# Kernel optimization log

Measured on AMD Instinct MI355X. Metric: run time of the kernel, lower is better.

## Reference

```python
import jax, jax.numpy as jnp
import numpy as np

N, E, H, FE, FV, L, FL, FO = 20000, 320000, 256, 64, 64, 4, 1024, 1


def setup_inputs() -> dict:
    key = jax.random.key(0)
    ks = jax.random.split(key, 28)
    s = 0.05
    rn = lambda k, shp: jax.random.normal(k, shp, jnp.float32) * s
    inp = {
        'x': jax.random.normal(ks[0], (N, FV), jnp.float32),
        'edge_attr': jax.random.normal(ks[1], (E, FE), jnp.float32),
        'edge_index': jax.random.randint(ks[2], (2, E), 0, N, jnp.int64) if False else jax.random.randint(ks[2], (2, E), 0, N),
        'ew': rn(ks[3], (H, FE)), 'eb': rn(ks[4], (H,)),
        'vw': rn(ks[5], (H, FV)), 'vb': rn(ks[6], (H,)),
        'Le_w': rn(ks[7], (L, H, H)), 'Le_b': rn(ks[8], (L, H)),
        'Lv_w': rn(ks[9], (L, H, H)), 'Lv_b': rn(ks[10], (L, H)),
        'bne_g': jnp.ones((L, H), jnp.float32), 'bne_b': jnp.zeros((L, H), jnp.float32),
        'bnv_g': jnp.ones((L, H), jnp.float32), 'bnv_b': jnp.zeros((L, H), jnp.float32),
        'gru_wih': rn(ks[11], (L, 3 * H, H)), 'gru_whh': rn(ks[12], (L, 3 * H, H)),
        'gru_bih': rn(ks[13], (L, 3 * H)), 'gru_bhh': rn(ks[14], (L, 3 * H)),
        'fin_w': rn(ks[15], (FL, H)), 'fin_b': rn(ks[16], (FL,)),
        'out_w': rn(ks[17], (FO, FL)), 'out_b': rn(ks[18], (FO,)),
    }
    return inp


def _bn(x, g, b):
    # BatchNorm1d, training-mode batch statistics (biased variance), eps=1e-5
    m = x.mean(axis=0)
    v = x.var(axis=0)
    return (x - m) * jax.lax.rsqrt(v + 1e-5) * g + b


def _forward(x, edge_attr, edge_index, ew, eb, vw, vb, Le_w, Le_b, Lv_w, Lv_b,
             bne_g, bne_b, bnv_g, bnv_b, gru_wih, gru_whh, gru_bih, gru_bhh,
             fin_w, fin_b, out_w, out_b):
    n_nodes = x.shape[0]
    num_layers = Le_w.shape[0]
    src, dst = edge_index[0], edge_index[1]
    seg = jnp.concatenate([src, dst])  # each edge contributes to both endpoints
    e_in = edge_attr @ ew.T + eb       # [E, H]
    v_in = x @ vw.T + vb               # [N, H]
    for k in range(num_layers):
        e = e_in @ Le_w[k].T + Le_b[k]
        vp = v_in @ Lv_w[k].T + Lv_b[k]
        ep = jax.nn.relu(_bn(e + vp[src] + vp[dst], bne_g[k], bne_b[k]))  # [E, H]
        # scatter-max of incident edge features into each vertex
        vie = jax.ops.segment_max(jnp.concatenate([ep, ep], axis=0), seg,
                                  num_segments=n_nodes)
        vie = jnp.where(jnp.isfinite(vie), vie, 0.0)  # isolated vertices -> 0
        # single-step GRU: input vie, hidden v_in
        gi = vie @ gru_wih[k].T + gru_bih[k]
        gh = v_in @ gru_whh[k].T + gru_bhh[k]
        ir, iz, ig = jnp.split(gi, 3, axis=1)
        hr, hz, hg = jnp.split(gh, 3, axis=1)
        r = jax.nn.sigmoid(ir + hr)
        z = jax.nn.sigmoid(iz + hz)
        n = jnp.tanh(ig + r * hg)
        h = (1.0 - z) * n + z * v_in
        v_c = jax.nn.relu(_bn(h, bnv_g[k], bnv_b[k]))
        v_in = v_c + v_in
        e_in = ep + e_in
    e_fin = e_in @ fin_w.T + fin_b
    return e_fin @ out_w.T + out_b  # [E, 1]


def reference(x, edge_attr, edge_index, ew, eb, vw, vb, Le_w, Le_b, Lv_w, Lv_b,
              bne_g, bne_b, bnv_g, bnv_b, gru_wih, gru_whh, gru_bih, gru_bhh,
              fin_w, fin_b, out_w, out_b):
    return _forward(x, edge_attr, edge_index, ew, eb, vw, vb, Le_w, Le_b, Lv_w,
                    Lv_b, bne_g, bne_b, bnv_g, bnv_b, gru_wih, gru_whh,
                    gru_bih, gru_bhh, fin_w, fin_b, out_w, out_b)
```

## Files before the change

### kernel.cpp

```cpp
#include <hip/hip_runtime.h>
#include <stdint.h>

constexpr int N  = 20000;
constexpr int E  = 320000;
constexpr int H  = 256;
constexpr int FEAT = 64;
constexpr int NL = 4;
constexpr int FL = 1024;

typedef unsigned short u16;
typedef short bf16x8 __attribute__((ext_vector_type(8)));
typedef float f32x4 __attribute__((ext_vector_type(4)));

__device__ __forceinline__ float bf2f(u16 u) {
    union { uint32_t i; float f; } v; v.i = ((uint32_t)u) << 16; return v.f;
}
__device__ __forceinline__ u16 f2bf(float f) {
    union { uint32_t i; float f; } v; v.f = f;
    uint32_t r = v.i + 0x7FFFu + ((v.i >> 16) & 1u);
    return (u16)(r >> 16);
}
__device__ __forceinline__ float sigmf(float x) { return 1.f / (1.f + __expf(-x)); }
__device__ __forceinline__ float tanhf_(float x) { return 2.f / (1.f + __expf(-2.f * x)) - 1.f; }

__device__ __forceinline__ unsigned int encf(float x) {
    unsigned int u = __float_as_uint(x);
    return (u & 0x80000000u) ? ~u : (u | 0x80000000u);
}
__device__ __forceinline__ float decf(unsigned int k) {
    unsigned int u = (k & 0x80000000u) ? (k ^ 0x80000000u) : ~k;
    return __uint_as_float(u);
}

template <bool W16>
__device__ __forceinline__ bf16x8 ldb(const u16* wb, const float* wf, size_t off) {
    if constexpr (W16) {
        return *(const bf16x8*)(wb + off);
    } else {
        float4 b0 = *(const float4*)(wf + off);
        float4 b1 = *(const float4*)(wf + off + 4);
        bf16x8 r;
        r[0] = (short)f2bf(b0.x); r[1] = (short)f2bf(b0.y);
        r[2] = (short)f2bf(b0.z); r[3] = (short)f2bf(b0.w);
        r[4] = (short)f2bf(b1.x); r[5] = (short)f2bf(b1.y);
        r[6] = (short)f2bf(b1.z); r[7] = (short)f2bf(b1.w);
        return r;
    }
}

__global__ void k_fuse_final(const float* __restrict__ fin_w, const float* __restrict__ fin_b,
                             const float* __restrict__ out_w, const float* __restrict__ out_b,
                             float* __restrict__ w_fo) {
    int h = threadIdx.x;
    float acc = 0.f;
    for (int f = 0; f < FL; ++f) acc = fmaf(out_w[f], fin_w[(size_t)f * H + h], acc);
    w_fo[h] = acc;
    if (h == 0) {
        float b = 0.f;
        for (int f = 0; f < FL; ++f) b = fmaf(out_w[f], fin_b[f], b);
        w_fo[H] = b + out_b[0];
    }
}

__global__ void k_cvt_w(const float* __restrict__ w, u16* __restrict__ o, int n4) {
    int i = blockIdx.x * 256 + threadIdx.x;
    if (i < n4) {
        float4 v = *(const float4*)(w + (size_t)i * 4);
        *(ushort4*)(o + (size_t)i * 4) = make_ushort4(f2bf(v.x), f2bf(v.y), f2bf(v.z), f2bf(v.w));
    }
}

__global__ void k_zero_int(int* __restrict__ p, int n) {
    int i = blockIdx.x * 256 + threadIdx.x;
    if (i < n) p[i] = 0;
}
__global__ void k_zero_f64(double* __restrict__ p, int n) {
    int i = blockIdx.x * 256 + threadIdx.x;
    if (i < n) p[i] = 0.0;
}
__global__ void k_hist2(const int* __restrict__ src, const int* __restrict__ dst,
                        int* __restrict__ curS, int* __restrict__ curD) {
    int e = blockIdx.x * 256 + threadIdx.x;
    if (e < E) { atomicAdd(&curS[src[e]], 1); atomicAdd(&curD[dst[e]], 1); }
}
__global__ void k_scan(int* __restrict__ cur) {
    __shared__ int cs[256];
    int t = threadIdx.x;
    constexpr int CH = (N + 255) / 256;
    int beg = t * CH, end = min(beg + CH, N);
    int s = 0;
    for (int i = beg; i < end; ++i) s += cur[i];
    cs[t] = s;
    __syncthreads();
    for (int off = 1; off < 256; off <<= 1) {
        int v = cs[t];
        int u = (t >= off) ? cs[t - off] : 0;
        __syncthreads();
        cs[t] = v + u;
        __syncthreads();
    }
    int run = (t > 0) ? cs[t - 1] : 0;
    for (int i = beg; i < end; ++i) { int d = cur[i]; cur[i] = run; run += d; }
}
__global__ void k_fill_pair(const int* __restrict__ src, const int* __restrict__ dst,
                            int* __restrict__ curS, int* __restrict__ curD,
                            int4* __restrict__ adjS, int4* __restrict__ adjD) {
    int e = blockIdx.x * 256 + threadIdx.x;
    if (e < E) {
        int s = src[e], d = dst[e];
        int p = atomicAdd(&curS[s], 1); adjS[p] = make_int4(e, s, d, s);
        int q = atomicAdd(&curD[d], 1); adjD[q] = make_int4(e, s, d, d);
    }
}
__global__ void k_fill_u32(unsigned int* __restrict__ p, unsigned int val) {
    size_t i = ((size_t)blockIdx.x * 256 + threadIdx.x) * 4;
    uint4 v = make_uint4(val, val, val, val);
    *(uint4*)(p + i) = v;
}

template <bool W16>
__global__ __launch_bounds__(256, 3) void k_proj_mfma(
    const float* __restrict__ A, const u16* __restrict__ wb, const float* __restrict__ wf,
    const float* __restrict__ bias, u16* __restrict__ C, int M)
{
    __shared__ u16 As[64][72];
    int t = threadIdx.x;
    int row0 = blockIdx.x * 64;
    int r = t >> 2, q = t & 3;
    if (row0 + r < M) {
        const float* gp = A + (size_t)(row0 + r) * FEAT + q * 16;
#pragma unroll
        for (int i = 0; i < 4; ++i) {
            float4 v = *(const float4*)(gp + i * 4);
            *(ushort4*)&As[r][q * 16 + i * 4] = make_ushort4(f2bf(v.x), f2bf(v.y), f2bf(v.z), f2bf(v.w));
        }
    } else {
#pragma unroll
        for (int i = 0; i < 4; ++i) *(ushort4*)&As[r][q * 16 + i * 4] = make_ushort4(0, 0, 0, 0);
    }
    __syncthreads();
    int w = t >> 6, l = t & 63, lane16 = l & 15, quad = l >> 4;
    f32x4 acc[4][4];
#pragma unroll
    for (int i = 0; i < 4; ++i)
#pragma unroll
        for (int j = 0; j < 4; ++j) acc[i][j] = (f32x4){0.f, 0.f, 0.f, 0.f};
#pragma unroll
    for (int k0 = 0; k0 < FEAT; k0 += 32) {
        bf16x8 a[4], b[4];
#pragma unroll
        for (int mt = 0; mt < 4; ++mt)
            a[mt] = *(const bf16x8*)&As[mt * 16 + lane16][k0 + quad * 8];
#pragma unroll
        for (int nt = 0; nt < 4; ++nt)
            b[nt] = ldb<W16>(wb, wf, (size_t)(w * 16 + nt * 64 + lane16) * FEAT + k0 + quad * 8);
#pragma unroll
        for (int mt = 0; mt < 4; ++mt)
#pragma unroll
            for (int nt = 0; nt < 4; ++nt)
                acc[mt][nt] = __builtin_amdgcn_mfma_f32_16x16x32_bf16(a[mt], b[nt], acc[mt][nt], 0, 0, 0);
    }
#pragma unroll
    for (int nt = 0; nt < 4; ++nt) {
        int col = w * 16 + nt * 64 + lane16;
        float bv = bias[col];
#pragma unroll
        for (int mt = 0; mt < 4; ++mt)
#pragma unroll
            for (int reg = 0; reg < 4; ++reg) {
                int row = mt * 16 + quad * 4 + reg;
                if (row0 + row < M)
                    C[(size_t)(row0 + row) * H + col] = f2bf(acc[mt][nt][reg] + bv);
            }
    }
}

template <bool W16>
__global__ __launch_bounds__(256, 2) void k_node_mfma(
    const u16* __restrict__ A, const u16* __restrict__ wb, const float* __restrict__ wf,
    u16* __restrict__ C)
{
    __shared__ u16 As[64][264];
    int t = threadIdx.x;
    int row0 = blockIdx.x * 64;
    int rows = min(64, N - row0);
    int r = t >> 2, q = t & 3;
    if (r < rows) {
        const u16* gp = A + (size_t)(row0 + r) * H + q * 64;
#pragma unroll
        for (int i = 0; i < 16; ++i)
            *(ushort4*)&As[r][q * 64 + i * 4] = *(const ushort4*)(gp + i * 4);
    } else {
#pragma unroll
        for (int i = 0; i < 16; ++i) *(ushort4*)&As[r][q * 64 + i * 4] = make_ushort4(0, 0, 0, 0);
    }
    __syncthreads();
    int w = t >> 6, l = t & 63, lane16 = l & 15, quad = l >> 4;
    f32x4 acc[4][4];
#pragma unroll
    for (int i = 0; i < 4; ++i)
#pragma unroll
        for (int j = 0; j < 4; ++j) acc[i][j] = (f32x4){0.f, 0.f, 0.f, 0.f};
    for (int k0 = 0; k0 < H; k0 += 32) {
        bf16x8 a[4], b[4];
#pragma unroll
        for (int mt = 0; mt < 4; ++mt)
            a[mt] = *(const bf16x8*)&As[mt * 16 + lane16][k0 + quad * 8];
#pragma unroll
        for (int nt = 0; nt < 4; ++nt)
            b[nt] = ldb<W16>(wb, wf, (size_t)(w * 16 + nt * 64 + lane16) * H + k0 + quad * 8);
#pragma unroll
        for (int mt = 0; mt < 4; ++mt)
#pragma unroll
            for (int nt = 0; nt < 4; ++nt)
                acc[mt][nt] = __builtin_amdgcn_mfma_f32_16x16x32_bf16(a[mt], b[nt], acc[mt][nt], 0, 0, 0);
    }
#pragma unroll
    for (int nt = 0; nt < 4; ++nt) {
        int col = w * 16 + nt * 64 + lane16;
#pragma unroll
        for (int mt = 0; mt < 4; ++mt)
#pragma unroll
            for (int reg = 0; reg < 4; ++reg) {
                int row = mt * 16 + quad * 4 + reg;
                if (row < rows)
                    C[(size_t)(row0 + row) * H + col] = f2bf(acc[mt][nt][reg]);
            }
    }
}

template <bool FIRST>
__global__ __launch_bounds__(256, 4) void k_edge_mfma(
    const u16* __restrict__ ein, const u16* __restrict__ wbf,
    const u16* __restrict__ vp, const int4* __restrict__ adj,
    const int* __restrict__ endo,
    unsigned int* __restrict__ vie, double* __restrict__ stats_e,
    const float* __restrict__ scale, const float* __restrict__ shift,
    u16* __restrict__ ein_rw)
{
    __shared__ u16 As[32][264];
    __shared__ u16 Us[32][264];
    __shared__ int s_edge[32];
    __shared__ int s_node[32];
    __shared__ int s_int[32];
    u16 (*praw)[264] = As;

    int t = threadIdx.x;
    int p0 = blockIdx.x * 32;
    if (t < 32) {
        int4 en = adj[p0 + t];
        s_edge[t] = en.x; s_node[t] = en.w;
        if (FIRST) {
            int nd = en.w;
            int st = (nd == 0) ? 0 : endo[nd - 1];
            int ee = endo[nd];
            s_int[t] = (st >= p0) && (ee <= p0 + 32);
        }
    }
    __syncthreads();
    int r = t >> 3, q = t & 7;
    {
        int4 en = adj[p0 + r];
        const u16* gp = ein + (size_t)en.x * H + q * 32;
        const u16* vs = vp + (size_t)en.y * H + q * 32;
        const u16* vd = vp + (size_t)en.z * H + q * 32;
#pragma unroll
        for (int i = 0; i < 8; ++i)
            *(ushort4*)&As[r][q * 32 + i * 4] = *(const ushort4*)(gp + i * 4);
#pragma unroll
        for (int i = 0; i < 8; ++i) {
            ushort4 a4 = *(const ushort4*)(vs + i * 4);
            ushort4 b4 = *(const ushort4*)(vd + i * 4);
            *(ushort4*)&Us[r][q * 32 + i * 4] = make_ushort4(
                f2bf(bf2f(a4.x) + bf2f(b4.x)), f2bf(bf2f(a4.y) + bf2f(b4.y)),
                f2bf(bf2f(a4.z) + bf2f(b4.z)), f2bf(bf2f(a4.w) + bf2f(b4.w)));
        }
    }
    __syncthreads();

    int w = t >> 6, l = t & 63, lane16 = l & 15, quad = l >> 4;
    f32x4 acc[2][4];
#pragma unroll
    for (int i = 0; i < 2; ++i)
#pragma unroll
        for (int j = 0; j < 4; ++j) acc[i][j] = (f32x4){0.f, 0.f, 0.f, 0.f};
    const u16* wb0 = wbf + (size_t)(w * 64 + lane16) * H + quad * 8;
    for (int k0 = 0; k0 < H; k0 += 32) {
        bf16x8 a[2], b[4];
#pragma unroll
        for (int mt = 0; mt < 2; ++mt)
            a[mt] = *(const bf16x8*)&As[mt * 16 + lane16][k0 + quad * 8];
#pragma unroll
        for (int nt = 0; nt < 4; ++nt)
            b[nt] = *(const bf16x8*)(wb0 + (size_t)nt * 16 * H + k0);
#pragma unroll
        for (int mt = 0; mt < 2; ++mt)
#pragma unroll
            for (int nt = 0; nt < 4; ++nt)
                acc[mt][nt] = __builtin_amdgcn_mfma_f32_16x16x32_bf16(a[mt], b[nt], acc[mt][nt], 0, 0, 0);
    }
    __syncthreads();

#pragma unroll
    for (int nt = 0; nt < 4; ++nt) {
        int col = w * 64 + nt * 16 + lane16;
        float s = 0.f, qq = 0.f;
#pragma unroll
        for (int mt = 0; mt < 2; ++mt)
#pragma unroll
            for (int reg = 0; reg < 4; ++reg) {
                int row = mt * 16 + quad * 4 + reg;
                float v = acc[mt][nt][reg] + bf2f(Us[row][col]);
                praw[row][col] = f2bf(v);
                if (FIRST) { s += v; qq += v * v; }
            }
        if (FIRST) {
            s  += __shfl_xor(s, 16, 64);  s  += __shfl_xor(s, 32, 64);
            qq += __shfl_xor(qq, 16, 64); qq += __shfl_xor(qq, 32, 64);
            if (quad == 0) {
                int slice = blockIdx.x & 63;
                atomicAdd(&stats_e[(size_t)slice * 512 + col], (double)s);
                atomicAdd(&stats_e[(size_t)slice * 512 + 256 + col], (double)qq);
            }
        }
    }
    __syncthreads();
    {
        int cur = s_node[0];
        float m = bf2f(praw[0][t]);
        for (int rr = 1; rr < 32; ++rr) {
            int nd = s_node[rr];
            float v = bf2f(praw[rr][t]);
            if (nd != cur) {
                if (FIRST && s_int[rr - 1])
                    vie[(size_t)cur * H + t] = encf(m);
                else
                    atomicMax(&vie[(size_t)cur * H + t], encf(m));
                cur = nd; m = v;
            } else m = fmaxf(m, v);
        }
        if (FIRST && s_int[31])
            vie[(size_t)cur * H + t] = encf(m);
        else
            atomicMax(&vie[(size_t)cur * H + t], encf(m));
    }
    if (!FIRST) {
        u16* gp = ein_rw + (size_t)s_edge[r] * H + q * 32;
        const float* scp = scale + q * 32;
        const float* shp = shift + q * 32;
#pragma unroll
        for (int i = 0; i < 8; ++i) {
            int c = q * 32 + i * 4;
            ushort2 pa = *(const ushort2*)&praw[r][c];
            ushort2 pb = *(const ushort2*)&praw[r][c + 2];
            float4 sc = *(const float4*)(scp + i * 4);
            float4 sh = *(const float4*)(shp + i * 4);
            ushort4 ev = *(const ushort4*)(gp + i * 4);
            float o0 = bf2f(ev.x) + fmaxf(fmaf(bf2f(pa.x), sc.x, sh.x), 0.f);
            float o1 = bf2f(ev.y) + fmaxf(fmaf(bf2f(pa.y), sc.y, sh.y), 0.f);
            float o2 = bf2f(ev.z) + fmaxf(fmaf(bf2f(pb.x), sc.z, sh.z), 0.f);
            float o3 = bf2f(ev.w) + fmaxf(fmaf(bf2f(pb.y), sc.w, sh.w), 0.f);
            *(ushort4*)(gp + i * 4) = make_ushort4(f2bf(o0), f2bf(o1), f2bf(o2), f2bf(o3));
        }
    }
}

__global__ void k_bn_final_e(const double* __restrict__ stats_e,
                             const float* __restrict__ g, const float* __restrict__ b,
                             float* __restrict__ scale, float* __restrict__ shift) {
    int j = threadIdx.x;
    double m = 0.0, q = 0.0;
    for (int s = 0; s < 64; ++s) {
        m += stats_e[(size_t)s * 512 + j];
        q += stats_e[(size_t)s * 512 + 256 + j];
    }
    m /= (double)E;
    double var = q / (double)E - m * m;
    if (var < 0.0) var = 0.0;
    float inv = rsqrtf((float)var + 1e-5f);
    float sc = g[j] * inv;
    scale[j] = sc;
    shift[j] = b[j] - (float)m * sc;
}

__global__ void k_bn_final(const double* __restrict__ stats, int base,
                           const float* __restrict__ g, const float* __restrict__ b,
                           double cnt, float* __restrict__ scale, float* __restrict__ shift) {
    int j = threadIdx.x;
    double m = stats[base + j] / cnt;
    double var = stats[base + 256 + j] / cnt - m * m;
    if (var < 0.0) var = 0.0;
    float inv = rsqrtf((float)var + 1e-5f);
    float sc = g[j] * inv;
    scale[j] = sc;
    shift[j] = b[j] - (float)m * sc;
}

__global__ void k_vie_final(unsigned int* __restrict__ vie_u,
                            const float* __restrict__ scale, const float* __restrict__ shift) {
    size_t idx = ((size_t)blockIdx.x * 256 + threadIdx.x) * 4;
    int col = (int)(idx & (size_t)(H - 1));
    uint4 u = *(const uint4*)(vie_u + idx);
    float4 sc = *(const float4*)(scale + col);
    float4 sh = *(const float4*)(shift + col);
    float4 o;
    o.x = (u.x == 0u) ? 0.f : fmaxf(fmaf(decf(u.x), sc.x, sh.x), 0.f);
    o.y = (u.y == 0u) ? 0.f : fmaxf(fmaf(decf(u.y), sc.y, sh.y), 0.f);
    o.z = (u.z == 0u) ? 0.f : fmaxf(fmaf(decf(u.z), sc.z, sh.z), 0.f);
    o.w = (u.w == 0u) ? 0.f : fmaxf(fmaf(decf(u.w), sc.w, sh.w), 0.f);
    *(float4*)((float*)vie_u + idx) = o;
}

template <bool W16>
__global__ __launch_bounds__(256, 2) void k_gru_mfma(
    const float* __restrict__ vie, const u16* __restrict__ vin,
    const u16* __restrict__ wihb, const float* __restrict__ wihf,
    const u16* __restrict__ whhb, const float* __restrict__ whhf,
    const float* __restrict__ bih, const float* __restrict__ bhh,
    u16* __restrict__ hout, double* __restrict__ stats_v)
{
    __shared__ u16 Ae[64][264];
    __shared__ u16 Av[64][264];
    __shared__ float csum[256], csq[256];
    int t = threadIdx.x;
    int row0 = blockIdx.x * 64;
    int rows = min(64, N - row0);
    int r = t >> 2, q = t & 3;
    if (r < rows) {
        const float* gp = vie + (size_t)(row0 + r) * H + q * 64;
        const u16* hp = vin + (size_t)(row0 + r) * H + q * 64;
#pragma unroll
        for (int i = 0; i < 16; ++i) {
            float4 v = *(const float4*)(gp + i * 4);
            *(ushort4*)&Ae[r][q * 64 + i * 4] = make_ushort4(f2bf(v.x), f2bf(v.y), f2bf(v.z), f2bf(v.w));
            *(ushort4*)&Av[r][q * 64 + i * 4] = *(const ushort4*)(hp + i * 4);
        }
    } else {
#pragma unroll
        for (int i = 0; i < 16; ++i) {
            *(ushort4*)&Ae[r][q * 64 + i * 4] = make_ushort4(0, 0, 0, 0);
            *(ushort4*)&Av[r][q * 64 + i * 4] = make_ushort4(0, 0, 0, 0);
        }
    }
    __syncthreads();
    int w = t >> 6, l = t & 63, lane16 = l & 15, quad = l >> 4;

    for (int g = 0; g < 4; ++g) {
        int j = g * 64 + w * 16 + lane16;
        f32x4 aR[4], aZ[4], aIG[4], aHG[4];
#pragma unroll
        for (int mt = 0; mt < 4; ++mt) {
            aR[mt] = (f32x4){0.f, 0.f, 0.f, 0.f};  aZ[mt] = (f32x4){0.f, 0.f, 0.f, 0.f};
            aIG[mt] = (f32x4){0.f, 0.f, 0.f, 0.f}; aHG[mt] = (f32x4){0.f, 0.f, 0.f, 0.f};
        }
        for (int k0 = 0; k0 < H; k0 += 32) {
            size_t kq = (size_t)k0 + quad * 8;
            bf16x8 ae[4], av[4];
#pragma unroll
            for (int mt = 0; mt < 4; ++mt) {
                ae[mt] = *(const bf16x8*)&Ae[mt * 16 + lane16][k0 + quad * 8];
                av[mt] = *(const bf16x8*)&Av[mt * 16 + lane16][k0 + quad * 8];
            }
            bf16x8 bri = ldb<W16>(wihb, wihf, (size_t)j * H + kq);
            bf16x8 bzi = ldb<W16>(wihb, wihf, (size_t)(H + j) * H + kq);
            bf16x8 bgi = ldb<W16>(wihb, wihf, (size_t)(2 * H + j) * H + kq);
            bf16x8 brh = ldb<W16>(whhb, whhf, (size_t)j * H + kq);
            bf16x8 bzh = ldb<W16>(whhb, whhf, (size_t)(H + j) * H + kq);
            bf16x8 bgh = ldb<W16>(whhb, whhf, (size_t)(2 * H + j) * H + kq);
#pragma unroll
            for (int mt = 0; mt < 4; ++mt) {
                aR[mt]  = __builtin_amdgcn_mfma_f32_16x16x32_bf16(ae[mt], bri, aR[mt], 0, 0, 0);
                aR[mt]  = __builtin_amdgcn_mfma_f32_16x16x32_bf16(av[mt], brh, aR[mt], 0, 0, 0);
                aZ[mt]  = __builtin_amdgcn_mfma_f32_16x16x32_bf16(ae[mt], bzi, aZ[mt], 0, 0, 0);
                aZ[mt]  = __builtin_amdgcn_mfma_f32_16x16x32_bf16(av[mt], bzh, aZ[mt], 0, 0, 0);
                aIG[mt] = __builtin_amdgcn_mfma_f32_16x16x32_bf16(ae[mt], bgi, aIG[mt], 0, 0, 0);
                aHG[mt] = __builtin_amdgcn_mfma_f32_16x16x32_bf16(av[mt], bgh, aHG[mt], 0, 0, 0);
            }
        }
        float br_ = bih[j] + bhh[j];
        float bz_ = bih[H + j] + bhh[H + j];
        float bgi_ = bih[2 * H + j];
        float bgh_ = bhh[2 * H + j];
        float s = 0.f, qq = 0.f;
#pragma unroll
        for (int mt = 0; mt < 4; ++mt)
#pragma unroll
            for (int reg = 0; reg < 4; ++reg) {
                int row = mt * 16 + quad * 4 + reg;
                float rr = sigmf(aR[mt][reg] + br_);
                float zz = sigmf(aZ[mt][reg] + bz_);
                float nn = tanhf_(aIG[mt][reg] + bgi_ + rr * (aHG[mt][reg] + bgh_));
                float vv = bf2f(Av[row][j]);
                float hv = (1.f - zz) * nn + zz * vv;
                if (row < rows) {
                    hout[(size_t)(row0 + row) * H + j] = f2bf(hv);
                    s += hv; qq += hv * hv;
                }
            }
        s  += __shfl_xor(s, 16, 64);  s  += __shfl_xor(s, 32, 64);
        qq += __shfl_xor(qq, 16, 64); qq += __shfl_xor(qq, 32, 64);
        if (quad == 0) { csum[j] = s; csq[j] = qq; }
    }
    __syncthreads();
    atomicAdd(&stats_v[t], (double)csum[t]);
    atomicAdd(&stats_v[256 + t], (double)csq[t]);
}

__global__ void k_vertex_update(u16* __restrict__ vin, const u16* __restrict__ h,
                                const float* __restrict__ scale, const float* __restrict__ shift) {
    size_t idx = ((size_t)blockIdx.x * 256 + threadIdx.x) * 4;
    int col = (int)(idx & (size_t)(H - 1));
    ushort4 hv = *(const ushort4*)(h + idx);
    float4 sc = *(const float4*)(scale + col);
    float4 sh = *(const float4*)(shift + col);
    ushort4 vv = *(const ushort4*)(vin + idx);
    float o0 = bf2f(vv.x) + fmaxf(fmaf(bf2f(hv.x), sc.x, sh.x), 0.f);
    float o1 = bf2f(vv.y) + fmaxf(fmaf(bf2f(hv.y), sc.y, sh.y), 0.f);
    float o2 = bf2f(vv.z) + fmaxf(fmaf(bf2f(hv.z), sc.z, sh.z), 0.f);
    float o3 = bf2f(vv.w) + fmaxf(fmaf(bf2f(hv.w), sc.w, sh.w), 0.f);
    *(ushort4*)(vin + idx) = make_ushort4(f2bf(o0), f2bf(o1), f2bf(o2), f2bf(o3));
}

__global__ __launch_bounds__(256) void k_final(const u16* __restrict__ ein,
                                               const float* __restrict__ w_fo, float* __restrict__ out) {
    int t = threadIdx.x;
    int lane = t & 63;
    int w = (blockIdx.x << 2) + (t >> 6);
    float4 wv = *(const float4*)(w_fo + lane * 4);
    float bfo = w_fo[H];
    int e0 = w * 64;
    for (int e = e0; e < e0 + 64; ++e) {
        ushort4 u = *(const ushort4*)(ein + (size_t)e * H + lane * 4);
        float p = bf2f(u.x) * wv.x + bf2f(u.y) * wv.y + bf2f(u.z) * wv.z + bf2f(u.w) * wv.w;
        for (int off = 32; off > 0; off >>= 1) p += __shfl_down(p, off, 64);
        if (lane == 0) out[e] = p + bfo;
    }
}

template <bool W16>
static void run_all(void* const* d_in, void* d_out, void* d_ws, hipStream_t stream) {
    const float* x         = (const float*)d_in[0];
    const float* edge_attr = (const float*)d_in[1];
    const int*   ei        = (const int*)d_in[2];
    const int*   src = ei;
    const int*   dst = ei + E;
    const float* ew  = (const float*)d_in[3];
    const float* eb  = (const float*)d_in[4];
    const float* vw  = (const float*)d_in[5];
    const float* vb  = (const float*)d_in[6];
    const float* Le_w = (const float*)d_in[7];
    const float* Lv_w = (const float*)d_in[9];
    const float* bne_g = (const float*)d_in[11];
    const float* bne_b = (const float*)d_in[12];
    const float* bnv_g = (const float*)d_in[13];
    const float* bnv_b = (const float*)d_in[14];
    const float* gwih  = (const float*)d_in[15];
    const float* gwhh  = (const float*)d_in[16];
    const float* gbih  = (const float*)d_in[17];
    const float* gbhh  = (const float*)d_in[18];
    const float* fin_w = (const float*)d_in[19];
    const float* fin_b = (const float*)d_in[20];
    const float* out_w = (const float*)d_in[21];
    const float* out_b = (const float*)d_in[22];
    float* out = (float*)d_out;

    const size_t nh = (size_t)N * H, eh = (size_t)E * H;
    char* base = (char*)d_ws;
    size_t off = 0;
    auto alloc = [&](size_t bytes) -> char* {
        char* p = base + off;
        off = (off + bytes + 255) & ~(size_t)255;
        return p;
    };
    float* w_fo = (float*)alloc((H + 1) * sizeof(float));
    u16* v_in = (u16*)alloc(nh * sizeof(u16));
    u16* vp   = (u16*)alloc(nh * sizeof(u16));
    unsigned int* vie_u = (unsigned int*)alloc(nh * sizeof(unsigned int));
    u16* e_in = (u16*)alloc(eh * sizeof(u16));
    u16* wbf  = (u16*)alloc((size_t)NL * H * H * sizeof(u16));
    double* stats_e = (double*)alloc((size_t)64 * 512 * sizeof(double));
    double* stats_v = (double*)alloc(512 * sizeof(double));
    float* scale_e = (float*)alloc(H * sizeof(float));
    float* shift_e = (float*)alloc(H * sizeof(float));
    float* scale_v = (float*)alloc(H * sizeof(float));
    float* shift_v = (float*)alloc(H * sizeof(float));
    int* curS = (int*)alloc((size_t)N * sizeof(int));
    int* curD = (int*)alloc((size_t)N * sizeof(int));
    int4* adjS = (int4*)alloc((size_t)E * sizeof(int4));
    int4* adjD = (int4*)alloc((size_t)E * sizeof(int4));
    u16 *wbf_v = nullptr, *wbf_ih = nullptr, *wbf_hh = nullptr, *ew_b = nullptr, *vw_b = nullptr;
    if (W16) {
        wbf_v  = (u16*)alloc((size_t)NL * H * H * sizeof(u16));
        wbf_ih = (u16*)alloc((size_t)NL * 3 * H * H * sizeof(u16));
        wbf_hh = (u16*)alloc((size_t)NL * 3 * H * H * sizeof(u16));
        ew_b   = (u16*)alloc((size_t)H * FEAT * sizeof(u16));
        vw_b   = (u16*)alloc((size_t)H * FEAT * sizeof(u16));
    }
    u16* hbuf = vp;

    k_fuse_final<<<1, 256, 0, stream>>>(fin_w, fin_b, out_w, out_b, w_fo);
    k_cvt_w<<<(NL * H * H / 4 + 255) / 256, 256, 0, stream>>>(Le_w, wbf, NL * H * H / 4);
    if (W16) {
        k_cvt_w<<<(NL * H * H / 4 + 255) / 256, 256, 0, stream>>>(Lv_w, wbf_v, NL * H * H / 4);
        k_cvt_w<<<(NL * 3 * H * H / 4 + 255) / 256, 256, 0, stream>>>(gwih, wbf_ih, NL * 3 * H * H / 4);
        k_cvt_w<<<(NL * 3 * H * H / 4 + 255) / 256, 256, 0, stream>>>(gwhh, wbf_hh, NL * 3 * H * H / 4);
        k_cvt_w<<<(H * FEAT / 4 + 255) / 256, 256, 0, stream>>>(ew, ew_b, H * FEAT / 4);
        k_cvt_w<<<(H * FEAT / 4 + 255) / 256, 256, 0, stream>>>(vw, vw_b, H * FEAT / 4);
    }
    k_zero_int<<<(N + 255) / 256, 256, 0, stream>>>(curS, N);
    k_zero_int<<<(N + 255) / 256, 256, 0, stream>>>(curD, N);
    k_hist2<<<E / 256, 256, 0, stream>>>(src, dst, curS, curD);
    k_scan<<<1, 256, 0, stream>>>(curS);
    k_scan<<<1, 256, 0, stream>>>(curD);
    k_fill_pair<<<E / 256, 256, 0, stream>>>(src, dst, curS, curD, adjS, adjD);
    const int ntile = (N + 63) / 64;
    k_proj_mfma<W16><<<ntile, 256, 0, stream>>>(x, vw_b, vw, vb, v_in, N);
    k_proj_mfma<W16><<<E / 64, 256, 0, stream>>>(edge_attr, ew_b, ew, eb, e_in, E);

    const int nstat = 64 * 512 + 512;
    for (int k = 0; k < NL; ++k) {
        k_zero_f64<<<(nstat + 255) / 256, 256, 0, stream>>>(stats_e, nstat);
        k_fill_u32<<<(int)(nh / 4 / 256), 256, 0, stream>>>(vie_u, 0u);
        k_node_mfma<W16><<<ntile, 256, 0, stream>>>(v_in,
            W16 ? wbf_v + (size_t)k * H * H : nullptr, Lv_w + (size_t)k * H * H, vp);
        k_edge_mfma<true><<<E / 32, 256, 0, stream>>>(e_in, wbf + (size_t)k * H * H, vp,
                                                      adjD, curD, vie_u, stats_e, nullptr, nullptr, nullptr);
        k_bn_final_e<<<1, 256, 0, stream>>>(stats_e, bne_g + k * H, bne_b + k * H, scale_e, shift_e);
        k_edge_mfma<false><<<E / 32, 256, 0, stream>>>(e_in, wbf + (size_t)k * H * H, vp,
                                                       adjS, curS, vie_u, nullptr, scale_e, shift_e, e_in);
        k_vie_final<<<(int)(nh / 4 / 256), 256, 0, stream>>>(vie_u, scale_e, shift_e);
        k_gru_mfma<W16><<<ntile, 256, 0, stream>>>((const float*)vie_u, v_in,
            W16 ? wbf_ih + (size_t)k * 3 * H * H : nullptr, gwih + (size_t)k * 3 * H * H,
            W16 ? wbf_hh + (size_t)k * 3 * H * H : nullptr, gwhh + (size_t)k * 3 * H * H,
            gbih + (size_t)k * 3 * H, gbhh + (size_t)k * 3 * H, hbuf, stats_v);
        k_bn_final<<<1, 256, 0, stream>>>(stats_v, 0, bnv_g + k * H, bnv_b + k * H, (double)N, scale_v, shift_v);
        k_vertex_update<<<(int)(nh / 4 / 256), 256, 0, stream>>>(v_in, hbuf, scale_v, shift_v);
    }
    k_final<<<E / 256, 256, 0, stream>>>(e_in, w_fo, out);
}

extern "C" void kernel_launch(void* const* d_in, const int* in_sizes, int n_in,
                              void* d_out, int out_size, void* d_ws, size_t ws_size,
                              hipStream_t stream) {
    (void)in_sizes; (void)n_in; (void)out_size;
    const size_t nh = (size_t)N * H, eh = (size_t)E * H;
    auto rup = [](size_t x) { return (x + 255) & ~(size_t)255; };
    size_t need_base = rup((H + 1) * 4) + 2 * rup(nh * 2) + rup(nh * 4) + rup(eh * 2)
                     + rup((size_t)NL * H * H * 2) + rup((size_t)64 * 512 * 8) + rup(512 * 8)
                     + 4 * rup(H * 4) + 2 * rup((size_t)N * 4) + 2 * rup((size_t)E * 16);
    size_t need_w16 = rup((size_t)NL * H * H * 2)
                    + 2 * rup((size_t)NL * 3 * H * H * 2) + 2 * rup((size_t)H * FEAT * 2);
    if (ws_size == 0 || ws_size >= need_base + need_w16)
        run_all<true>(d_in, d_out, d_ws, stream);
    else
        run_all<false>(d_in, d_out, d_ws, stream);
}
```

Baseline: 2.984 ms.

## Store edge features permuted in destination-sorted order for coalesced access

Edge features e_in are now stored in dst-sorted order: the initial projection scatters rows through a permutation, and the first edge pass reads its tiles contiguously instead of gathering by edge id. The second (src-sorted) pass indexes through the permuted position, and the final output kernel scatters results back to original edge order. This removes one random gather per layer in the first pass and drops the separate adjD table, in exchange for a permuted write at projection time and a scattered final output write.

New measurement: 3.030 ms. About the same (+1.5%).

```diff
diff --git a/kernel.cpp b/kernel.cpp
--- a/kernel.cpp
+++ b/kernel.cpp
@@ -7,6 +7,7 @@
 constexpr int FEAT = 64;
 constexpr int NL = 4;
 constexpr int FL = 1024;
+constexpr int NB_E = E / 32;
 
 typedef unsigned short u16;
 typedef short bf16x8 __attribute__((ext_vector_type(8)));
@@ -102,14 +103,17 @@
     int run = (t > 0) ? cs[t - 1] : 0;
     for (int i = beg; i < end; ++i) { int d = cur[i]; cur[i] = run; run += d; }
 }
-__global__ void k_fill_pair(const int* __restrict__ src, const int* __restrict__ dst,
+__global__ void k_fill_perm(const int* __restrict__ src, const int* __restrict__ dst,
                             int* __restrict__ curS, int* __restrict__ curD,
-                            int4* __restrict__ adjS, int4* __restrict__ adjD) {
+                            int4* __restrict__ adjS, int4* __restrict__ sd2, int* __restrict__ pos) {
     int e = blockIdx.x * 256 + threadIdx.x;
     if (e < E) {
         int s = src[e], d = dst[e];
-        int p = atomicAdd(&curS[s], 1); adjS[p] = make_int4(e, s, d, s);
-        int q = atomicAdd(&curD[d], 1); adjD[q] = make_int4(e, s, d, d);
+        int q = atomicAdd(&curD[d], 1);
+        sd2[q] = make_int4(s, d, e, 0);
+        pos[e] = q;
+        int p = atomicAdd(&curS[s], 1);
+        adjS[p] = make_int4(q, s, d, s);
     }
 }
 __global__ void k_fill_u32(unsigned int* __restrict__ p, unsigned int val) {
@@ -121,7 +125,7 @@
 template <bool W16>
 __global__ __launch_bounds__(256, 3) void k_proj_mfma(
     const float* __restrict__ A, const u16* __restrict__ wb, const float* __restrict__ wf,
-    const float* __restrict__ bias, u16* __restrict__ C, int M)
+    const float* __restrict__ bias, u16* __restrict__ C, int M, const int* __restrict__ perm)
 {
     __shared__ u16 As[64][72];
     int t = threadIdx.x;
@@ -169,8 +173,10 @@
 #pragma unroll
             for (int reg = 0; reg < 4; ++reg) {
                 int row = mt * 16 + quad * 4 + reg;
-                if (row0 + row < M)
-                    C[(size_t)(row0 + row) * H + col] = f2bf(acc[mt][nt][reg] + bv);
+                if (row0 + row < M) {
+                    int pr = perm ? perm[row0 + row] : row0 + row;
+                    C[(size_t)pr * H + col] = f2bf(acc[mt][nt][reg] + bv);
+                }
             }
     }
 }
@@ -229,41 +235,26 @@
     }
 }
 
-template <bool FIRST>
-__global__ __launch_bounds__(256, 4) void k_edge_mfma(
-    const u16* __restrict__ ein, const u16* __restrict__ wbf,
-    const u16* __restrict__ vp, const int4* __restrict__ adj,
+__global__ __launch_bounds__(256, 4) void k_edge_first(
+    const u16* __restrict__ ein2, const u16* __restrict__ wbf,
+    const u16* __restrict__ vp, const int4* __restrict__ sd2,
     const int* __restrict__ endo,
-    unsigned int* __restrict__ vie, double* __restrict__ stats_e,
-    const float* __restrict__ scale, const float* __restrict__ shift,
-    u16* __restrict__ ein_rw)
+    unsigned int* __restrict__ vie, double* __restrict__ stats_e)
 {
     __shared__ u16 As[32][264];
     __shared__ u16 Us[32][264];
-    __shared__ int s_edge[32];
     __shared__ int s_node[32];
     __shared__ int s_int[32];
     u16 (*praw)[264] = As;
 
     int t = threadIdx.x;
     int p0 = blockIdx.x * 32;
-    if (t < 32) {
-        int4 en = adj[p0 + t];
-        s_edge[t] = en.x; s_node[t] = en.w;
-        if (FIRST) {
-            int nd = en.w;
-            int st = (nd == 0) ? 0 : endo[nd - 1];
-            int ee = endo[nd];
-            s_int[t] = (st >= p0) && (ee <= p0 + 32);
-        }
-    }
-    __syncthreads();
     int r = t >> 3, q = t & 7;
     {
-        int4 en = adj[p0 + r];
-        const u16* gp = ein + (size_t)en.x * H + q * 32;
-        const u16* vs = vp + (size_t)en.y * H + q * 32;
-        const u16* vd = vp + (size_t)en.z * H + q * 32;
+        int4 en = sd2[p0 + r];
+        const u16* gp = ein2 + (size_t)(p0 + r) * H + q * 32;
+        const u16* vs = vp + (size_t)en.x * H + q * 32;
+        const u16* vd = vp + (size_t)en.y * H + q * 32;
 #pragma unroll
         for (int i = 0; i < 8; ++i)
             *(ushort4*)&As[r][q * 32 + i * 4] = *(const ushort4*)(gp + i * 4);
@@ -276,6 +267,13 @@
                 f2bf(bf2f(a4.z) + bf2f(b4.z)), f2bf(bf2f(a4.w) + bf2f(b4.w)));
         }
     }
+    if (t < 32) {
+        int nd = sd2[p0 + t].y;
+        s_node[t] = nd;
+        int st = (nd == 0) ? 0 : endo[nd - 1];
+        int ee = endo[nd];
+        s_int[t] = (st >= p0) && (ee <= p0 + 32);
+    }
     __syncthreads();
 
     int w = t >> 6, l = t & 63, lane16 = l & 15, quad = l >> 4;
@@ -312,16 +310,14 @@
                 int row = mt * 16 + quad * 4 + reg;
                 float v = acc[mt][nt][reg] + bf2f(Us[row][col]);
                 praw[row][col] = f2bf(v);
-                if (FIRST) { s += v; qq += v * v; }
+                s += v; qq += v * v;
             }
-        if (FIRST) {
-            s  += __shfl_xor(s, 16, 64);  s  += __shfl_xor(s, 32, 64);
-            qq += __shfl_xor(qq, 16, 64); qq += __shfl_xor(qq, 32, 64);
-            if (quad == 0) {
-                int slice = blockIdx.x & 63;
-                atomicAdd(&stats_e[(size_t)slice * 512 + col], (double)s);
-                atomicAdd(&stats_e[(size_t)slice * 512 + 256 + col], (double)qq);
-            }
+        s  += __shfl_xor(s, 16, 64);  s  += __shfl_xor(s, 32, 64);
+        qq += __shfl_xor(qq, 16, 64); qq += __shfl_xor(qq, 32, 64);
+        if (quad == 0) {
+            int slice = blockIdx.x & 63;
+            atomicAdd(&stats_e[(size_t)slice * 512 + col], (double)s);
+            atomicAdd(&stats_e[(size_t)slice * 512 + 256 + col], (double)qq);
         }
     }
     __syncthreads();
@@ -332,20 +328,105 @@
             int nd = s_node[rr];
             float v = bf2f(praw[rr][t]);
             if (nd != cur) {
-                if (FIRST && s_int[rr - 1])
-                    vie[(size_t)cur * H + t] = encf(m);
-                else
-                    atomicMax(&vie[(size_t)cur * H + t], encf(m));
+                if (s_int[rr - 1]) vie[(size_t)cur * H + t] = encf(m);
+                else atomicMax(&vie[(size_t)cur * H + t], encf(m));
                 cur = nd; m = v;
             } else m = fmaxf(m, v);
         }
-        if (FIRST && s_int[31])
-            vie[(size_t)cur * H + t] = encf(m);
-        else
-            atomicMax(&vie[(size_t)cur * H + t], encf(m));
-    }
-    if (!FIRST) {
-        u16* gp = ein_rw + (size_t)s_edge[r] * H + q * 32;
+        if (s_int[31]) vie[(size_t)cur * H + t] = encf(m);
+        else atomicMax(&vie[(size_t)cur * H + t], encf(m));
+    }
+}
+
+__global__ __launch_bounds__(256, 4) void k_edge_second(
+    const u16* __restrict__ ein2, const u16* __restrict__ wbf,
+    const u16* __restrict__ vp, const int4* __restrict__ adj,
+    unsigned int* __restrict__ vie,
+    const float* __restrict__ scale, const float* __restrict__ shift,
+    u16* __restrict__ ein_rw)
+{
+    __shared__ u16 As[32][264];
+    __shared__ u16 Us[32][264];
+    __shared__ int s_pos[32];
+    __shared__ int s_node[32];
+    u16 (*praw)[264] = As;
+
+    int t = threadIdx.x;
+    int p0 = blockIdx.x * 32;
+    int r = t >> 3, q = t & 7;
+    {
+        int4 en = adj[p0 + r];
+        const u16* gp = ein2 + (size_t)en.x * H + q * 32;
+        const u16* vs = vp + (size_t)en.y * H + q * 32;
+        const u16* vd = vp + (size_t)en.z * H + q * 32;
+#pragma unroll
+        for (int i = 0; i < 8; ++i)
+            *(ushort4*)&As[r][q * 32 + i * 4] = *(const ushort4*)(gp + i * 4);
+#pragma unroll
+        for (int i = 0; i < 8; ++i) {
+            ushort4 a4 = *(const ushort4*)(vs + i * 4);
+            ushort4 b4 = *(const ushort4*)(vd + i * 4);
+            *(ushort4*)&Us[r][q * 32 + i * 4] = make_ushort4(
+                f2bf(bf2f(a4.x) + bf2f(b4.x)), f2bf(bf2f(a4.y) + bf2f(b4.y)),
+                f2bf(bf2f(a4.z) + bf2f(b4.z)), f2bf(bf2f(a4.w) + bf2f(b4.w)));
+        }
+    }
+    if (t < 32) {
+        int4 en = adj[p0 + t];
+        s_pos[t] = en.x; s_node[t] = en.w;
+    }
+    __syncthreads();
+
+    int w = t >> 6, l = t & 63, lane16 = l & 15, quad = l >> 4;
+    f32x4 acc[2][4];
+#pragma unroll
+    for (int i = 0; i < 2; ++i)
+#pragma unroll
+        for (int j = 0; j < 4; ++j) acc[i][j] = (f32x4){0.f, 0.f, 0.f, 0.f};
+    const u16* wb0 = wbf + (size_t)(w * 64 + lane16) * H + quad * 8;
+    for (int k0 = 0; k0 < H; k0 += 32) {
+        bf16x8 a[2], b[4];
+#pragma unroll
+        for (int mt = 0; mt < 2; ++mt)
+            a[mt] = *(const bf16x8*)&As[mt * 16 + lane16][k0 + quad * 8];
+#pragma unroll
+        for (int nt = 0; nt < 4; ++nt)
+            b[nt] = *(const bf16x8*)(wb0 + (size_t)nt * 16 * H + k0);
+#pragma unroll
+        for (int mt = 0; mt < 2; ++mt)
+#pragma unroll
+            for (int nt = 0; nt < 4; ++nt)
+                acc[mt][nt] = __builtin_amdgcn_mfma_f32_16x16x32_bf16(a[mt], b[nt], acc[mt][nt], 0, 0, 0);
+    }
+    __syncthreads();
+
+#pragma unroll
+    for (int nt = 0; nt < 4; ++nt) {
+        int col = w * 64 + nt * 16 + lane16;
+#pragma unroll
+        for (int mt = 0; mt < 2; ++mt)
+#pragma unroll
+            for (int reg = 0; reg < 4; ++reg) {
+                int row = mt * 16 + quad * 4 + reg;
+                praw[row][col] = f2bf(acc[mt][nt][reg] + bf2f(Us[row][col]));
+            }
+    }
+    __syncthreads();
+    {
+        int cur = s_node[0];
+        float m = bf2f(praw[0][t]);
+        for (int rr = 1; rr < 32; ++rr) {
+            int nd = s_node[rr];
+            float v = bf2f(praw[rr][t]);
+            if (nd != cur) {
+                atomicMax(&vie[(size_t)cur * H + t], encf(m));
+                cur = nd; m = v;
+            } else m = fmaxf(m, v);
+        }
+        atomicMax(&vie[(size_t)cur * H + t], encf(m));
+    }
+    {
+        u16* gp = ein_rw + (size_t)s_pos[r] * H + q * 32;
         const float* scp = scale + q * 32;
         const float* shp = shift + q * 32;
 #pragma unroll
@@ -521,19 +602,20 @@
     *(ushort4*)(vin + idx) = make_ushort4(f2bf(o0), f2bf(o1), f2bf(o2), f2bf(o3));
 }
 
-__global__ __launch_bounds__(256) void k_final(const u16* __restrict__ ein,
+__global__ __launch_bounds__(256) void k_final(const u16* __restrict__ ein2,
+                                               const int4* __restrict__ sd2,
                                                const float* __restrict__ w_fo, float* __restrict__ out) {
     int t = threadIdx.x;
     int lane = t & 63;
     int w = (blockIdx.x << 2) + (t >> 6);
     float4 wv = *(const float4*)(w_fo + lane * 4);
     float bfo = w_fo[H];
-    int e0 = w * 64;
-    for (int e = e0; e < e0 + 64; ++e) {
-        ushort4 u = *(const ushort4*)(ein + (size_t)e * H + lane * 4);
-        float p = bf2f(u.x) * wv.x + bf2f(u.y) * wv.y + bf2f(u.z) * wv.z + bf2f(u.w) * wv.w;
-        for (int off = 32; off > 0; off >>= 1) p += __shfl_down(p, off, 64);
-        if (lane == 0) out[e] = p + bfo;
+    int p0 = w * 64;
+    for (int p = p0; p < p0 + 64; ++p) {
+        ushort4 u = *(const ushort4*)(ein2 + (size_t)p * H + lane * 4);
+        float s = bf2f(u.x) * wv.x + bf2f(u.y) * wv.y + bf2f(u.z) * wv.z + bf2f(u.w) * wv.w;
+        for (int off = 32; off > 0; off >>= 1) s += __shfl_down(s, off, 64);
+        if (lane == 0) out[sd2[p].z] = s + bfo;
     }
 }
 
@@ -587,7 +669,8 @@
     int* curS = (int*)alloc((size_t)N * sizeof(int));
     int* curD = (int*)alloc((size_t)N * sizeof(int));
     int4* adjS = (int4*)alloc((size_t)E * sizeof(int4));
-    int4* adjD = (int4*)alloc((size_t)E * sizeof(int4));
+    int4* sd2  = (int4*)alloc((size_t)E * sizeof(int4));
+    int*  pos  = (int*)alloc((size_t)E * sizeof(int));
     u16 *wbf_v = nullptr, *wbf_ih = nullptr, *wbf_hh = nullptr, *ew_b = nullptr, *vw_b = nullptr;
     if (W16) {
         wbf_v  = (u16*)alloc((size_t)NL * H * H * sizeof(u16));
@@ -612,10 +695,10 @@
     k_hist2<<<E / 256, 256, 0, stream>>>(src, dst, curS, curD);
     k_scan<<<1, 256, 0, stream>>>(curS);
     k_scan<<<1, 256, 0, stream>>>(curD);
-    k_fill_pair<<<E / 256, 256, 0, stream>>>(src, dst, curS, curD, adjS, adjD);
+    k_fill_perm<<<E / 256, 256, 0, stream>>>(src, dst, curS, curD, adjS, sd2, pos);
     const int ntile = (N + 63) / 64;
-    k_proj_mfma<W16><<<ntile, 256, 0, stream>>>(x, vw_b, vw, vb, v_in, N);
-    k_proj_mfma<W16><<<E / 64, 256, 0, stream>>>(edge_attr, ew_b, ew, eb, e_in, E);
+    k_proj_mfma<W16><<<ntile, 256, 0, stream>>>(x, vw_b, vw, vb, v_in, N, nullptr);
+    k_proj_mfma<W16><<<E / 64, 256, 0, stream>>>(edge_attr, ew_b, ew, eb, e_in, E, pos);
 
     const int nstat = 64 * 512 + 512;
     for (int k = 0; k < NL; ++k) {
@@ -623,11 +706,11 @@
         k_fill_u32<<<(int)(nh / 4 / 256), 256, 0, stream>>>(vie_u, 0u);
         k_node_mfma<W16><<<ntile, 256, 0, stream>>>(v_in,
             W16 ? wbf_v + (size_t)k * H * H : nullptr, Lv_w + (size_t)k * H * H, vp);
-        k_edge_mfma<true><<<E / 32, 256, 0, stream>>>(e_in, wbf + (size_t)k * H * H, vp,
-                                                      adjD, curD, vie_u, stats_e, nullptr, nullptr, nullptr);
+        k_edge_first<<<NB_E, 256, 0, stream>>>(e_in, wbf + (size_t)k * H * H, vp,
+                                               sd2, curD, vie_u, stats_e);
         k_bn_final_e<<<1, 256, 0, stream>>>(stats_e, bne_g + k * H, bne_b + k * H, scale_e, shift_e);
-        k_edge_mfma<false><<<E / 32, 256, 0, stream>>>(e_in, wbf + (size_t)k * H * H, vp,
-                                                       adjS, curS, vie_u, nullptr, scale_e, shift_e, e_in);
+        k_edge_second<<<NB_E, 256, 0, stream>>>(e_in, wbf + (size_t)k * H * H, vp,
+                                                adjS, vie_u, scale_e, shift_e, e_in);
         k_vie_final<<<(int)(nh / 4 / 256), 256, 0, stream>>>(vie_u, scale_e, shift_e);
         k_gru_mfma<W16><<<ntile, 256, 0, stream>>>((const float*)vie_u, v_in,
             W16 ? wbf_ih + (size_t)k * 3 * H * H : nullptr, gwih + (size_t)k * 3 * H * H,
@@ -636,7 +719,7 @@
         k_bn_final<<<1, 256, 0, stream>>>(stats_v, 0, bnv_g + k * H, bnv_b + k * H, (double)N, scale_v, shift_v);
         k_vertex_update<<<(int)(nh / 4 / 256), 256, 0, stream>>>(v_in, hbuf, scale_v, shift_v);
     }
-    k_final<<<E / 256, 256, 0, stream>>>(e_in, w_fo, out);
+    k_final<<<E / 256, 256, 0, stream>>>(e_in, sd2, w_fo, out);
 }
 
 extern "C" void kernel_launch(void* const* d_in, const int* in_sizes, int n_in,
@@ -647,7 +730,8 @@
     auto rup = [](size_t x) { return (x + 255) & ~(size_t)255; };
     size_t need_base = rup((H + 1) * 4) + 2 * rup(nh * 2) + rup(nh * 4) + rup(eh * 2)
                      + rup((size_t)NL * H * H * 2) + rup((size_t)64 * 512 * 8) + rup(512 * 8)
-                     + 4 * rup(H * 4) + 2 * rup((size_t)N * 4) + 2 * rup((size_t)E * 16);
+                     + 4 * rup(H * 4) + 2 * rup((size_t)N * 4) + 2 * rup((size_t)E * 16)
+                     + rup((size_t)E * 4);
     size_t need_w16 = rup((size_t)NL * H * H * 2)
                     + 2 * rup((size_t)NL * 3 * H * H * 2) + 2 * rup((size_t)H * FEAT * 2);
     if (ws_size == 0 || ws_size >= need_base + need_w16)
```
